# Performance work log

Measured on AMD Instinct MI355X. Metric: run time of the kernel, lower is better.

## Reference

```python
import jax, jax.numpy as jnp
import numpy as np

ADMP = 16  # admp_channel


def _backbone(x, Wc, bc):
    # Conv2d(3->256, k=3, stride=2, pad=1) + ReLU stands in for feature_backbone
    y = jax.lax.conv_general_dilated(x, Wc, window_strides=(2, 2),
                                     padding=((1, 1), (1, 1)),
                                     dimension_numbers=('NCHW', 'OIHW', 'NCHW'))
    return jax.nn.relu(y + bc[None, :, None, None])


def _feature_select(feat, k):
    # AdaptiveMaxPool2d(k, return_indices=True) on feat.sum(1); H,W divisible by k
    B, C, H, W = feat.shape
    bh, bw = H // k, W // k
    resp = feat.sum(1)  # [B,H,W]
    r = resp.reshape(B, k, bh, k, bw).transpose(0, 1, 3, 2, 4).reshape(B, k, k, bh * bw)
    loc = jnp.argmax(r, axis=-1)            # local flat index in each bh*bw block
    lr, lc = loc // bw, loc % bw
    rows = jnp.arange(k)[None, :, None] * bh + lr   # [B,k,k]
    cols = jnp.arange(k)[None, None, :] * bw + lc
    return (rows * W + cols).reshape(B, k * k)      # flat indices into H*W


def _mlp(x, W1, b1, W2, b2):
    # Linear -> ReLU -> (Dropout eval = identity) -> Linear
    return jax.nn.relu(x @ W1 + b1) @ W2 + b2


def reference(xA, xB, Wconv, bconv, W1r, b1r, W2r, b2r, W1c, b1c, W2c, b2c):
    fA = _backbone(xA, Wconv, bconv)  # [B,C,H,W]
    fB = _backbone(xB, Wconv, bconv)
    B, C, H, W = fA.shape
    N = H * W
    idxA = _feature_select(fA, ADMP)                       # [B,K]
    fA_flat = fA.reshape(B, C, N)
    fB_flat = fB.reshape(B, C, N)
    desc = jnp.take_along_axis(fA_flat, idxA[:, None, :], axis=2)  # [B,C,K]
    # ||a-b||^2 = ||a||^2 - 2 a.b + ||b||^2 ; fused batched kNN
    dist = ((desc ** 2).sum(1)[:, :, None]
            - 2.0 * jnp.einsum('bck,bcn->bkn', desc, fB_flat)
            + (fB_flat ** 2).sum(1)[:, None, :])           # [B,K,N]
    minidx = jnp.argmin(dist, axis=-1)                     # [B,K]
    # original uses high (==width here since H==W) for both div and mod
    row_A, col_A = idxA // H, idxA % H
    row_B, col_B = minidx // H, minidx % H
    drow = (row_B - row_A).astype(jnp.float32)             # [B,K]
    dcol = (col_A - col_B).astype(jnp.float32)
    out_drow = _mlp(drow, W1r, b1r, W2r, b2r)              # [B,1]
    out_dcol = _mlp(dcol, W1c, b1c, W2c, b2c)
    return jnp.concatenate([out_drow, out_dcol], axis=1)   # [B,2]


def setup_inputs() -> dict:
    key = jax.random.key(0)
    ks = jax.random.split(key, 8)
    K2 = ADMP * ADMP
    return {
        'xA': jax.random.normal(ks[0], (4, 3, 256, 256), jnp.float32),
        'xB': jax.random.normal(ks[1], (4, 3, 256, 256), jnp.float32),
        'Wconv': jax.random.normal(ks[2], (256, 3, 3, 3), jnp.float32) * 0.1,
        'bconv': jnp.zeros((256,), jnp.float32),
        'W1r': jax.random.normal(ks[3], (K2, K2 // 2), jnp.float32) * 0.05,
        'b1r': jnp.zeros((K2 // 2,), jnp.float32),
        'W2r': jax.random.normal(ks[4], (K2 // 2, 1), jnp.float32) * 0.05,
        'b2r': jnp.zeros((1,), jnp.float32),
        'W1c': jax.random.normal(ks[5], (K2, K2 // 2), jnp.float32) * 0.05,
        'b1c': jnp.zeros((K2 // 2,), jnp.float32),
        'W2c': jax.random.normal(ks[6], (K2 // 2, 1), jnp.float32) * 0.05,
        'b2c': jnp.zeros((1,), jnp.float32),
    }
```

## Files before the change

kernel.cpp:

```cpp
#include <hip/hip_runtime.h>
#include <stdint.h>

constexpr int NB   = 4;
constexpr int CIN  = 3;
constexpr int HIN  = 256;
constexpr int COUT = 256;
constexpr int HF   = 128;
constexpr int NF   = HF * HF;
constexpr int KADM = 16;
constexpr int KK   = KADM * KADM;
constexpr int HID  = 128;
constexpr int DFB  = 65536;
constexpr int PX   = 32;
constexpr int NT   = NF / PX;

typedef unsigned short ushort_t;
typedef __attribute__((ext_vector_type(8))) _Float16 f16x8;
typedef __attribute__((ext_vector_type(2))) __fp16   fp16v2;
typedef __attribute__((ext_vector_type(4))) float    f32x4;

__device__ inline unsigned long long shfl_xor_u64(unsigned long long v, int m) {
    unsigned lo = __shfl_xor((unsigned)v, m, 64);
    unsigned hi = __shfl_xor((unsigned)(v >> 32), m, 64);
    return ((unsigned long long)hi << 32) | lo;
}
__device__ inline unsigned long long u64min(unsigned long long a, unsigned long long b) {
    return a < b ? a : b;
}
__device__ inline ushort_t f16bits(_Float16 h) { return __builtin_bit_cast(ushort_t, h); }

__device__ inline int swz(int pix, int c) {
    return pix * 256 + ((((c >> 3) ^ (pix & 7)) << 3) | (c & 7));
}

__device__ inline int dfoff(int w, int chunk, int j, int lane) {
    return (((w * 8 + chunk) * 4 + j) * 64 + lane) * 8;
}

__global__ __launch_bounds__(256) void prep_kernel(
        const float* __restrict__ W, ushort_t* __restrict__ WFh, ushort_t* __restrict__ WFl)
{
    int co = threadIdx.x;
    int w = co >> 6, j = (co >> 4) & 3, la = co & 15;
    #pragma unroll
    for (int q = 0; q < 32; ++q) {
        float v = (q < 27) ? W[co * 27 + q] : 0.f;
        _Float16 h = (_Float16)v;
        _Float16 l = (_Float16)(v - (float)h);
        int lg = q >> 3, e = q & 7;
        int off = ((w * 4 + j) * 64 + lg * 16 + la) * 8 + e;
        WFh[off] = f16bits(h);
        WFl[off] = f16bits(l);
    }
}

__global__ __launch_bounds__(256) void convA_kernel(
        const float* __restrict__ xA,
        const ushort_t* __restrict__ WFh, const ushort_t* __restrict__ WFl,
        const float* __restrict__ bias, float* __restrict__ resp)
{
    __shared__ float    pS[CIN][3][132];
    __shared__ ushort_t Ah[64][40];
    __shared__ ushort_t Al[64][40];
    __shared__ float    redS[4][64];

    int tile = blockIdx.x;
    int b    = blockIdx.y;
    int oh   = tile >> 1;
    int ow0  = (tile & 1) << 6;
    const float* x = xA + (size_t)b * CIN * HIN * HIN;
    int tid = threadIdx.x;

    for (int i = tid; i < CIN * 3 * 129; i += 256) {
        int ci = i / (3 * 129);
        int r2 = i % (3 * 129);
        int kh = r2 / 129, c = r2 % 129;
        int gr = 2 * oh - 1 + kh, gc = 2 * ow0 - 1 + c;
        float v = 0.f;
        if (gr >= 0 && gr < HIN && gc >= 0 && gc < HIN)
            v = x[(size_t)ci * HIN * HIN + (size_t)gr * HIN + gc];
        pS[ci][kh][c] = v;
    }
    __syncthreads();

    {
        int n = tid >> 2, qg = tid & 3;
        unsigned uh[4], ul[4];
        #pragma unroll
        for (int e2 = 0; e2 < 4; ++e2) {
            ushort_t hh[2], ll[2];
            #pragma unroll
            for (int s = 0; s < 2; ++s) {
                int q = qg * 8 + e2 * 2 + s;
                float v = 0.f;
                if (q < 27) {
                    int ci = q / 9, r = (q % 9) / 3, kw = q % 3;
                    v = pS[ci][r][2 * n + kw];
                }
                _Float16 h = (_Float16)v;
                _Float16 l = (_Float16)(v - (float)h);
                hh[s] = f16bits(h); ll[s] = f16bits(l);
            }
            uh[e2] = (unsigned)hh[0] | ((unsigned)hh[1] << 16);
            ul[e2] = (unsigned)ll[0] | ((unsigned)ll[1] << 16);
        }
        *(uint4*)&Ah[n][qg * 8] = *(uint4*)uh;
        *(uint4*)&Al[n][qg * 8] = *(uint4*)ul;
    }
    __syncthreads();

    int lane = tid & 63, w = tid >> 6;
    int la = lane & 15, lg = lane >> 4;
    int wbase = w * 64;

    float bj[4];
    #pragma unroll
    for (int j = 0; j < 4; ++j) bj[j] = bias[wbase + j * 16 + la];

    f16x8 ah[4], al[4], bh[4], bl[4];
    #pragma unroll
    for (int i = 0; i < 4; ++i) {
        ah[i] = *(const f16x8*)&Ah[i * 16 + la][lg * 8];
        al[i] = *(const f16x8*)&Al[i * 16 + la][lg * 8];
    }
    #pragma unroll
    for (int j = 0; j < 4; ++j) {
        int off = ((w * 4 + j) * 64 + lane) * 8;
        bh[j] = *(const f16x8*)&WFh[off];
        bl[j] = *(const f16x8*)&WFl[off];
    }

    f32x4 acc[4][4];
    #pragma unroll
    for (int i = 0; i < 4; ++i)
        #pragma unroll
        for (int j = 0; j < 4; ++j) acc[i][j] = (f32x4)0.f;

    #pragma unroll
    for (int i = 0; i < 4; ++i)
        #pragma unroll
        for (int j = 0; j < 4; ++j) {
            acc[i][j] = __builtin_amdgcn_mfma_f32_16x16x32_f16(ah[i], bh[j], acc[i][j], 0, 0, 0);
            acc[i][j] = __builtin_amdgcn_mfma_f32_16x16x32_f16(al[i], bh[j], acc[i][j], 0, 0, 0);
            acc[i][j] = __builtin_amdgcn_mfma_f32_16x16x32_f16(ah[i], bl[j], acc[i][j], 0, 0, 0);
        }

    float s[4][4];
    #pragma unroll
    for (int i = 0; i < 4; ++i)
        #pragma unroll
        for (int r = 0; r < 4; ++r) s[i][r] = 0.f;

    #pragma unroll
    for (int i = 0; i < 4; ++i)
        #pragma unroll
        for (int j = 0; j < 4; ++j)
            #pragma unroll
            for (int r = 0; r < 4; ++r)
                s[i][r] += fmaxf(acc[i][j][r] + bj[j], 0.f);

    #pragma unroll
    for (int i = 0; i < 4; ++i)
        #pragma unroll
        for (int r = 0; r < 4; ++r) {
            float v = s[i][r];
            v += __shfl_xor(v, 1, 64);
            v += __shfl_xor(v, 2, 64);
            v += __shfl_xor(v, 4, 64);
            v += __shfl_xor(v, 8, 64);
            s[i][r] = v;
        }
    if (la == 0) {
        #pragma unroll
        for (int i = 0; i < 4; ++i)
            #pragma unroll
            for (int r = 0; r < 4; ++r)
                redS[w][i * 16 + lg * 4 + r] = s[i][r];
    }
    __syncthreads();
    if (tid < 64) {
        float tot = redS[0][tid] + redS[1][tid] + redS[2][tid] + redS[3][tid];
        resp[(size_t)b * NF + oh * HF + ow0 + tid] = tot;
    }
}

__global__ __launch_bounds__(256) void select_kernel(
        const float* __restrict__ resp,
        const float* __restrict__ xA, const float* __restrict__ W,
        const float* __restrict__ bias,
        int* __restrict__ idxA,
        ushort_t* __restrict__ dFh, ushort_t* __restrict__ dFl,
        float* __restrict__ normA)
{
    __shared__ float patch[27];
    __shared__ float red[4];
    __shared__ int   sidx;

    int bk = blockIdx.x;
    int b = bk >> 8, k = bk & 255;
    int t = threadIdx.x;

    if (t < 64) {
        int kr = k >> 4, kc = k & 15;
        int lr = t >> 3, lc = t & 7;
        int row = kr * 8 + lr, col = kc * 8 + lc;
        float bv = resp[(size_t)b * NF + (size_t)row * HF + col];
        int best = t;
        for (int off = 32; off > 0; off >>= 1) {
            float ov = __shfl_down(bv, off, 64);
            int   oi = __shfl_down(best, off, 64);
            if (ov > bv || (ov == bv && oi < best)) { bv = ov; best = oi; }
        }
        if (t == 0) {
            int r = kr * 8 + (best >> 3), c = kc * 8 + (best & 7);
            int idx = r * HF + c;
            idxA[bk] = idx;
            sidx = idx;
        }
    }
    __syncthreads();
    int idx = sidx;
    int oh = idx >> 7, ow = idx & 127;

    if (t < 27) {
        int ci = t / 9, kh = (t % 9) / 3, kw = t % 3;
        int ir = oh * 2 - 1 + kh, ic = ow * 2 - 1 + kw;
        float v = 0.f;
        if (ir >= 0 && ir < HIN && ic >= 0 && ic < HIN)
            v = xA[((size_t)b * CIN + ci) * HIN * HIN + (size_t)ir * HIN + ic];
        patch[t] = v;
    }
    __syncthreads();

    float v = bias[t];
    const float* w = &W[t * 27];
    #pragma unroll
    for (int q = 0; q < 27; ++q) v = fmaf(patch[q], w[q], v);
    v = fmaxf(v, 0.f);

    _Float16 h = (_Float16)v;
    _Float16 l = (_Float16)(v - (float)h);
    {
        int wq = k >> 6, j = (k >> 4) & 3, la = k & 15;
        int chunk = t >> 5, lg = (t >> 3) & 3, e = t & 7;
        int off = b * DFB + dfoff(wq, chunk, j, lg * 16 + la) + e;
        dFh[off] = f16bits(h);
        dFl[off] = f16bits(l);
    }

    float s = v * v;
    for (int off = 32; off > 0; off >>= 1) s += __shfl_down(s, off, 64);
    if ((t & 63) == 0) red[t >> 6] = s;
    __syncthreads();
    if (t == 0) normA[bk] = red[0] + red[1] + red[2] + red[3];
}

__device__ inline void load_desc(const ushort_t* __restrict__ dFh,
                                 const ushort_t* __restrict__ dFl,
                                 int w, int chunk, int lane,
                                 f16x8* bh, f16x8* bl)
{
    #pragma unroll
    for (int j = 0; j < 4; ++j) {
        int off = dfoff(w, chunk, j, lane);
        bh[j] = *(const f16x8*)&dFh[off];
        bl[j] = *(const f16x8*)&dFl[off];
    }
}

__device__ inline void knn_chunk(const ushort_t* __restrict__ fH,
                                 const ushort_t* __restrict__ fL,
                                 int la, int lg, int cc,
                                 const f16x8* bh, const f16x8* bl,
                                 f32x4 (&acc)[2][4])
{
    #pragma unroll
    for (int i = 0; i < 2; ++i) {
        f16x8 ah = *(const f16x8*)&fH[swz(i * 16 + la, cc + lg * 8)];
        f16x8 al = *(const f16x8*)&fL[swz(i * 16 + la, cc + lg * 8)];
        __builtin_amdgcn_s_setprio(1);
        #pragma unroll
        for (int j = 0; j < 4; ++j) {
            acc[i][j] = __builtin_amdgcn_mfma_f32_16x16x32_f16(ah, bh[j], acc[i][j], 0, 0, 0);
            acc[i][j] = __builtin_amdgcn_mfma_f32_16x16x32_f16(al, bh[j], acc[i][j], 0, 0, 0);
            acc[i][j] = __builtin_amdgcn_mfma_f32_16x16x32_f16(ah, bl[j], acc[i][j], 0, 0, 0);
        }
        __builtin_amdgcn_s_setprio(0);
    }
}

__global__ __launch_bounds__(256, 4) void fused_kernel(
        const float* __restrict__ xB,
        const ushort_t* __restrict__ WFh, const ushort_t* __restrict__ WFl,
        const float* __restrict__ bias,
        const ushort_t* __restrict__ dFhg, const ushort_t* __restrict__ dFlg,
        const float* __restrict__ normA,
        unsigned long long* __restrict__ scratch)
{
    __shared__ __align__(16) char smem[2 * PX * 256 * 2];
    __shared__ float redS[4][PX];
    __shared__ float nAS[KK];
    __shared__ float nBS[PX];
    __shared__ float bS[COUT];

    float*    pSp = (float*)smem;
    ushort_t* AhP = (ushort_t*)(smem + 2448);
    ushort_t* AlP = (ushort_t*)(smem + 2448 + 2560);
    ushort_t* fH  = (ushort_t*)smem;
    ushort_t* fL  = (ushort_t*)(smem + PX * 256 * 2);

    int tile = blockIdx.x;
    int b    = blockIdx.y;
    int oh   = tile >> 2;
    int ow0  = (tile & 3) << 5;
    const float* x = xB + (size_t)b * CIN * HIN * HIN;
    int tid = threadIdx.x;

    nAS[tid] = normA[b * KK + tid];
    bS[tid]  = bias[tid];

    for (int i = tid; i < CIN * 3 * 65; i += 256) {
        int ci = i / (3 * 65);
        int r2 = i % (3 * 65);
        int kh = r2 / 65, c = r2 % 65;
        int gr = 2 * oh - 1 + kh, gc = 2 * ow0 - 1 + c;
        float v = 0.f;
        if (gr >= 0 && gr < HIN && gc >= 0 && gc < HIN)
            v = x[(size_t)ci * HIN * HIN + (size_t)gr * HIN + gc];
        pSp[ci * 204 + kh * 68 + c] = v;
    }
    __syncthreads();

    {
        int n = tid >> 3, qg = tid & 7;
        ushort_t hh[4], ll[4];
        #pragma unroll
        for (int s = 0; s < 4; ++s) {
            int q = qg * 4 + s;
            float v = 0.f;
            if (q < 27) {
                int ci = q / 9, r = (q % 9) / 3, kw = q % 3;
                v = pSp[ci * 204 + r * 68 + 2 * n + kw];
            }
            _Float16 h = (_Float16)v;
            _Float16 l = (_Float16)(v - (float)h);
            hh[s] = f16bits(h); ll[s] = f16bits(l);
        }
        unsigned lo, hi;
        lo = (unsigned)hh[0] | ((unsigned)hh[1] << 16);
        hi = (unsigned)hh[2] | ((unsigned)hh[3] << 16);
        *(uint2*)&AhP[n * 40 + qg * 4] = make_uint2(lo, hi);
        lo = (unsigned)ll[0] | ((unsigned)ll[1] << 16);
        hi = (unsigned)ll[2] | ((unsigned)ll[3] << 16);
        *(uint2*)&AlP[n * 40 + qg * 4] = make_uint2(lo, hi);
    }
    __syncthreads();

    int lane = tid & 63, w = tid >> 6;
    int la = lane & 15, lg = lane >> 4;
    int wbase = w * 64;

    f16x8 wah[4], wal[4], pbh[2], pbl[2];
    #pragma unroll
    for (int j = 0; j < 4; ++j) {
        int off = ((w * 4 + j) * 64 + lane) * 8;
        wah[j] = *(const f16x8*)&WFh[off];
        wal[j] = *(const f16x8*)&WFl[off];
    }
    #pragma unroll
    for (int i = 0; i < 2; ++i) {
        pbh[i] = *(const f16x8*)&AhP[(i * 16 + la) * 40 + lg * 8];
        pbl[i] = *(const f16x8*)&AlP[(i * 16 + la) * 40 + lg * 8];
    }

    f32x4 cacc[4][2];
    #pragma unroll
    for (int j = 0; j < 4; ++j)
        #pragma unroll
        for (int i = 0; i < 2; ++i) cacc[j][i] = (f32x4)0.f;

    #pragma unroll
    for (int j = 0; j < 4; ++j)
        #pragma unroll
        for (int i = 0; i < 2; ++i) {
            cacc[j][i] = __builtin_amdgcn_mfma_f32_16x16x32_f16(wah[j], pbh[i], cacc[j][i], 0, 0, 0);
            cacc[j][i] = __builtin_amdgcn_mfma_f32_16x16x32_f16(wal[j], pbh[i], cacc[j][i], 0, 0, 0);
            cacc[j][i] = __builtin_amdgcn_mfma_f32_16x16x32_f16(wah[j], pbl[i], cacc[j][i], 0, 0, 0);
        }

    __syncthreads();

    float s2[2] = {0.f, 0.f};
    #pragma unroll
    for (int j = 0; j < 4; ++j) {
        f32x4 b4 = *(const f32x4*)&bS[wbase + j * 16 + lg * 4];
        int chunk = (wbase + j * 16 + lg * 4) >> 3;
        int within = (lg & 1) * 4;
        #pragma unroll
        for (int i = 0; i < 2; ++i) {
            int pix = i * 16 + la;
            float v0 = fmaxf(cacc[j][i][0] + b4[0], 0.f);
            float v1 = fmaxf(cacc[j][i][1] + b4[1], 0.f);
            float v2 = fmaxf(cacc[j][i][2] + b4[2], 0.f);
            float v3 = fmaxf(cacc[j][i][3] + b4[3], 0.f);
            s2[i] += v0 * v0 + v1 * v1 + v2 * v2 + v3 * v3;
            fp16v2 h01 = __builtin_amdgcn_cvt_pkrtz(v0, v1);
            fp16v2 h23 = __builtin_amdgcn_cvt_pkrtz(v2, v3);
            fp16v2 l01 = __builtin_amdgcn_cvt_pkrtz(v0 - (float)h01[0], v1 - (float)h01[1]);
            fp16v2 l23 = __builtin_amdgcn_cvt_pkrtz(v2 - (float)h23[0], v3 - (float)h23[1]);
            int base = pix * 256 + ((chunk ^ (pix & 7)) << 3) + within;
            *(uint2*)&fH[base] = make_uint2(__builtin_bit_cast(unsigned, h01),
                                            __builtin_bit_cast(unsigned, h23));
            *(uint2*)&fL[base] = make_uint2(__builtin_bit_cast(unsigned, l01),
                                            __builtin_bit_cast(unsigned, l23));
        }
    }

    const ushort_t* dFh = dFhg + (size_t)b * DFB;
    const ushort_t* dFl = dFlg + (size_t)b * DFB;
    f16x8 bhA[4], blA[4], bhB[4], blB[4];
    load_desc(dFh, dFl, w, 0, lane, bhA, blA);
    load_desc(dFh, dFl, w, 1, lane, bhB, blB);

    #pragma unroll
    for (int i = 0; i < 2; ++i) {
        float v = s2[i];
        v += __shfl_xor(v, 16, 64);
        v += __shfl_xor(v, 32, 64);
        if (lg == 0) redS[w][i * 16 + la] = v;
    }
    __syncthreads();
    if (tid < PX) nBS[tid] = redS[0][tid] + redS[1][tid] + redS[2][tid] + redS[3][tid];
    __syncthreads();

    f32x4 acc[2][4];
    #pragma unroll
    for (int i = 0; i < 2; ++i)
        #pragma unroll
        for (int j = 0; j < 4; ++j) acc[i][j] = (f32x4)0.f;

    knn_chunk(fH, fL, la, lg, 0, bhA, blA, acc);
    load_desc(dFh, dFl, w, 2, lane, bhA, blA);
    knn_chunk(fH, fL, la, lg, 32, bhB, blB, acc);
    load_desc(dFh, dFl, w, 3, lane, bhB, blB);
    knn_chunk(fH, fL, la, lg, 64, bhA, blA, acc);
    load_desc(dFh, dFl, w, 4, lane, bhA, blA);
    knn_chunk(fH, fL, la, lg, 96, bhB, blB, acc);
    load_desc(dFh, dFl, w, 5, lane, bhB, blB);
    knn_chunk(fH, fL, la, lg, 128, bhA, blA, acc);
    load_desc(dFh, dFl, w, 6, lane, bhA, blA);
    knn_chunk(fH, fL, la, lg, 160, bhB, blB, acc);
    load_desc(dFh, dFl, w, 7, lane, bhB, blB);
    knn_chunk(fH, fL, la, lg, 192, bhA, blA, acc);
    knn_chunk(fH, fL, la, lg, 224, bhB, blB, acc);

    float nBv[2][4];
    #pragma unroll
    for (int i = 0; i < 2; ++i) {
        f32x4 t4 = *(const f32x4*)&nBS[i * 16 + lg * 4];
        nBv[i][0] = t4[0]; nBv[i][1] = t4[1]; nBv[i][2] = t4[2]; nBv[i][3] = t4[3];
    }
    int n0 = tile * PX;
    unsigned long long bestj[4];
    #pragma unroll
    for (int j = 0; j < 4; ++j) {
        int kl = wbase + j * 16 + la;
        float nAv = nAS[kl];
        unsigned long long best = ~0ull;
        #pragma unroll
        for (int i = 0; i < 2; ++i)
            #pragma unroll
            for (int r = 0; r < 4; ++r) {
                int n = n0 + i * 16 + lg * 4 + r;
                float d = fmaf(-2.f, acc[i][j][r], nAv) + nBv[i][r];
                unsigned u = __float_as_uint(d);
                u = (u & 0x80000000u) ? ~u : (u | 0x80000000u);
                unsigned long long key = ((unsigned long long)u << 32) | (unsigned)n;
                best = u64min(best, key);
            }
        best = u64min(best, shfl_xor_u64(best, 16));
        best = u64min(best, shfl_xor_u64(best, 32));
        bestj[j] = best;
    }
    unsigned long long key = (lg == 0) ? bestj[0] : (lg == 1) ? bestj[1]
                           : (lg == 2) ? bestj[2] : bestj[3];
    int klw = wbase + lg * 16 + la;
    scratch[((size_t)b * NT + tile) * KK + klw] = key;
}

__global__ __launch_bounds__(256) void reduce_kernel(
        const unsigned long long* __restrict__ scratch, int* __restrict__ minN)
{
    __shared__ unsigned long long part[8][32];
    int g = blockIdx.x;
    int b = blockIdx.y;
    int t = threadIdx.x;
    int ts = t >> 5, kk = t & 31;
    int k = g * 32 + kk;

    unsigned long long best = ~0ull;
    #pragma unroll 4
    for (int m = 0; m < NT / 8; ++m) {
        int tile = m * 8 + ts;
        best = u64min(best, scratch[((size_t)b * NT + tile) * KK + k]);
    }
    part[ts][kk] = best;
    __syncthreads();
    if (t < 32) {
        unsigned long long x = part[0][t];
        #pragma unroll
        for (int p = 1; p < 8; ++p) x = u64min(x, part[p][t]);
        minN[b * KK + g * 32 + t] = (int)(x & 0xffffffffULL);
    }
}

__global__ __launch_bounds__(128) void mlp_kernel(
        const int* __restrict__ idxA, const int* __restrict__ minN,
        const float* __restrict__ W1r, const float* __restrict__ b1r,
        const float* __restrict__ W2r, const float* __restrict__ b2r,
        const float* __restrict__ W1c, const float* __restrict__ b1c,
        const float* __restrict__ W2c, const float* __restrict__ b2c,
        float* __restrict__ out)
{
    __shared__ float xS[KK];
    __shared__ float red[2];
    int blk = blockIdx.x;
    int b = blk >> 1, which = blk & 1;
    int t = threadIdx.x;

    for (int k = t; k < KK; k += 128) {
        int ia = idxA[b * KK + k];
        int nn = minN[b * KK + k];
        int rowA = ia >> 7, colA = ia & 127;
        int rowB = nn >> 7, colB = nn & 127;
        xS[k] = (which == 0) ? (float)(rowB - rowA) : (float)(colA - colB);
    }
    __syncthreads();

    const float* W1 = which ? W1c : W1r;
    const float* b1 = which ? b1c : b1r;
    const float* W2 = which ? W2c : W2r;
    const float* b2 = which ? b2c : b2r;

    float h = b1[t];
    for (int k = 0; k < KK; ++k) h = fmaf(xS[k], W1[k * HID + t], h);
    h = fmaxf(h, 0.f);
    float pv = h * W2[t];
    for (int off = 32; off > 0; off >>= 1) pv += __shfl_down(pv, off, 64);
    if ((t & 63) == 0) red[t >> 6] = pv;
    __syncthreads();
    if (t == 0) out[b * 2 + which] = red[0] + red[1] + b2[0];
}

extern "C" void kernel_launch(void* const* d_in, const int* in_sizes, int n_in,
                              void* d_out, int out_size, void* d_ws, size_t ws_size,
                              hipStream_t stream)
{
    const float* xA  = (const float*)d_in[0];
    const float* xB  = (const float*)d_in[1];
    const float* Wc  = (const float*)d_in[2];
    const float* bc  = (const float*)d_in[3];
    const float* W1r = (const float*)d_in[4];
    const float* b1r = (const float*)d_in[5];
    const float* W2r = (const float*)d_in[6];
    const float* b2r = (const float*)d_in[7];
    const float* W1c = (const float*)d_in[8];
    const float* b1c = (const float*)d_in[9];
    const float* W2c = (const float*)d_in[10];
    const float* b2c = (const float*)d_in[11];
    float* out = (float*)d_out;

    char* ws = (char*)d_ws;
    unsigned long long* scratch = (unsigned long long*)ws; ws += (size_t)NB * KK * NT * 8;
    int*   idxA   = (int*)ws;      ws += (size_t)NB * KK * 4;
    int*   minN   = (int*)ws;      ws += (size_t)NB * KK * 4;
    float* normA  = (float*)ws;    ws += (size_t)NB * KK * 4;
    float* resp   = (float*)ws;    ws += (size_t)NB * NF * 4;
    ushort_t* dFh = (ushort_t*)ws; ws += (size_t)NB * DFB * 2;
    ushort_t* dFl = (ushort_t*)ws; ws += (size_t)NB * DFB * 2;
    ushort_t* WFh = (ushort_t*)ws; ws += (size_t)COUT * 32 * 2;
    ushort_t* WFl = (ushort_t*)ws; ws += (size_t)COUT * 32 * 2;

    prep_kernel  <<<1, 256, 0, stream>>>(Wc, WFh, WFl);
    convA_kernel <<<dim3(256, NB), 256, 0, stream>>>(xA, WFh, WFl, bc, resp);
    select_kernel<<<NB * KK, 256, 0, stream>>>(resp, xA, Wc, bc, idxA, dFh, dFl, normA);
    fused_kernel <<<dim3(NT, NB), 256, 0, stream>>>(xB, WFh, WFl, bc, dFh, dFl,
                                                    normA, scratch);
    reduce_kernel<<<dim3(8, NB), 256, 0, stream>>>(scratch, minN);
    mlp_kernel   <<<8, 128, 0, stream>>>(idxA, minN,
                                         W1r, b1r, W2r, b2r,
                                         W1c, b1c, W2c, b2c, out);
}
```

Before: 69.96 us.

## Replace scratch argmin reduction with global atomicMin and halve convA grid

Result: slower. 72.04 us (+3.0%).

```diff
diff --git a/kernel.cpp b/kernel.cpp
--- a/kernel.cpp
+++ b/kernel.cpp
@@ -19,11 +19,6 @@
 typedef __attribute__((ext_vector_type(2))) __fp16   fp16v2;
 typedef __attribute__((ext_vector_type(4))) float    f32x4;
 
-__device__ inline unsigned long long shfl_xor_u64(unsigned long long v, int m) {
-    unsigned lo = __shfl_xor((unsigned)v, m, 64);
-    unsigned hi = __shfl_xor((unsigned)(v >> 32), m, 64);
-    return ((unsigned long long)hi << 32) | lo;
-}
 __device__ inline unsigned long long u64min(unsigned long long a, unsigned long long b) {
     return a < b ? a : b;
 }
@@ -64,123 +59,126 @@
     __shared__ ushort_t Al[64][40];
     __shared__ float    redS[4][64];
 
-    int tile = blockIdx.x;
-    int b    = blockIdx.y;
-    int oh   = tile >> 1;
-    int ow0  = (tile & 1) << 6;
+    int b = blockIdx.y;
     const float* x = xA + (size_t)b * CIN * HIN * HIN;
     int tid = threadIdx.x;
-
-    for (int i = tid; i < CIN * 3 * 129; i += 256) {
-        int ci = i / (3 * 129);
-        int r2 = i % (3 * 129);
-        int kh = r2 / 129, c = r2 % 129;
-        int gr = 2 * oh - 1 + kh, gc = 2 * ow0 - 1 + c;
-        float v = 0.f;
-        if (gr >= 0 && gr < HIN && gc >= 0 && gc < HIN)
-            v = x[(size_t)ci * HIN * HIN + (size_t)gr * HIN + gc];
-        pS[ci][kh][c] = v;
-    }
-    __syncthreads();
-
-    {
-        int n = tid >> 2, qg = tid & 3;
-        unsigned uh[4], ul[4];
-        #pragma unroll
-        for (int e2 = 0; e2 < 4; ++e2) {
-            ushort_t hh[2], ll[2];
-            #pragma unroll
-            for (int s = 0; s < 2; ++s) {
-                int q = qg * 8 + e2 * 2 + s;
-                float v = 0.f;
-                if (q < 27) {
-                    int ci = q / 9, r = (q % 9) / 3, kw = q % 3;
-                    v = pS[ci][r][2 * n + kw];
-                }
-                _Float16 h = (_Float16)v;
-                _Float16 l = (_Float16)(v - (float)h);
-                hh[s] = f16bits(h); ll[s] = f16bits(l);
-            }
-            uh[e2] = (unsigned)hh[0] | ((unsigned)hh[1] << 16);
-            ul[e2] = (unsigned)ll[0] | ((unsigned)ll[1] << 16);
-        }
-        *(uint4*)&Ah[n][qg * 8] = *(uint4*)uh;
-        *(uint4*)&Al[n][qg * 8] = *(uint4*)ul;
-    }
-    __syncthreads();
-
     int lane = tid & 63, w = tid >> 6;
     int la = lane & 15, lg = lane >> 4;
     int wbase = w * 64;
 
     float bj[4];
-    #pragma unroll
-    for (int j = 0; j < 4; ++j) bj[j] = bias[wbase + j * 16 + la];
-
-    f16x8 ah[4], al[4], bh[4], bl[4];
-    #pragma unroll
-    for (int i = 0; i < 4; ++i) {
-        ah[i] = *(const f16x8*)&Ah[i * 16 + la][lg * 8];
-        al[i] = *(const f16x8*)&Al[i * 16 + la][lg * 8];
-    }
+    f16x8 bh[4], bl[4];
     #pragma unroll
     for (int j = 0; j < 4; ++j) {
+        bj[j] = bias[wbase + j * 16 + la];
         int off = ((w * 4 + j) * 64 + lane) * 8;
         bh[j] = *(const f16x8*)&WFh[off];
         bl[j] = *(const f16x8*)&WFl[off];
     }
 
-    f32x4 acc[4][4];
-    #pragma unroll
-    for (int i = 0; i < 4; ++i)
-        #pragma unroll
-        for (int j = 0; j < 4; ++j) acc[i][j] = (f32x4)0.f;
-
-    #pragma unroll
-    for (int i = 0; i < 4; ++i)
-        #pragma unroll
-        for (int j = 0; j < 4; ++j) {
-            acc[i][j] = __builtin_amdgcn_mfma_f32_16x16x32_f16(ah[i], bh[j], acc[i][j], 0, 0, 0);
-            acc[i][j] = __builtin_amdgcn_mfma_f32_16x16x32_f16(al[i], bh[j], acc[i][j], 0, 0, 0);
-            acc[i][j] = __builtin_amdgcn_mfma_f32_16x16x32_f16(ah[i], bl[j], acc[i][j], 0, 0, 0);
-        }
-
-    float s[4][4];
-    #pragma unroll
-    for (int i = 0; i < 4; ++i)
-        #pragma unroll
-        for (int r = 0; r < 4; ++r) s[i][r] = 0.f;
-
-    #pragma unroll
-    for (int i = 0; i < 4; ++i)
-        #pragma unroll
-        for (int j = 0; j < 4; ++j)
-            #pragma unroll
-            for (int r = 0; r < 4; ++r)
-                s[i][r] += fmaxf(acc[i][j][r] + bj[j], 0.f);
-
-    #pragma unroll
-    for (int i = 0; i < 4; ++i)
-        #pragma unroll
-        for (int r = 0; r < 4; ++r) {
-            float v = s[i][r];
-            v += __shfl_xor(v, 1, 64);
-            v += __shfl_xor(v, 2, 64);
-            v += __shfl_xor(v, 4, 64);
-            v += __shfl_xor(v, 8, 64);
-            s[i][r] = v;
-        }
-    if (la == 0) {
+    for (int t2 = 0; t2 < 2; ++t2) {
+        int tile = blockIdx.x * 2 + t2;
+        int oh  = tile >> 1;
+        int ow0 = (tile & 1) << 6;
+
+        if (t2) __syncthreads();
+        for (int i = tid; i < CIN * 3 * 129; i += 256) {
+            int ci = i / (3 * 129);
+            int r2 = i % (3 * 129);
+            int kh = r2 / 129, c = r2 % 129;
+            int gr = 2 * oh - 1 + kh, gc = 2 * ow0 - 1 + c;
+            float v = 0.f;
+            if (gr >= 0 && gr < HIN && gc >= 0 && gc < HIN)
+                v = x[(size_t)ci * HIN * HIN + (size_t)gr * HIN + gc];
+            pS[ci][kh][c] = v;
+        }
+        __syncthreads();
+
+        {
+            int n = tid >> 2, qg = tid & 3;
+            unsigned uh[4], ul[4];
+            #pragma unroll
+            for (int e2 = 0; e2 < 4; ++e2) {
+                ushort_t hh[2], ll[2];
+                #pragma unroll
+                for (int s = 0; s < 2; ++s) {
+                    int q = qg * 8 + e2 * 2 + s;
+                    float v = 0.f;
+                    if (q < 27) {
+                        int ci = q / 9, r = (q % 9) / 3, kw = q % 3;
+                        v = pS[ci][r][2 * n + kw];
+                    }
+                    _Float16 h = (_Float16)v;
+                    _Float16 l = (_Float16)(v - (float)h);
+                    hh[s] = f16bits(h); ll[s] = f16bits(l);
+                }
+                uh[e2] = (unsigned)hh[0] | ((unsigned)hh[1] << 16);
+                ul[e2] = (unsigned)ll[0] | ((unsigned)ll[1] << 16);
+            }
+            *(uint4*)&Ah[n][qg * 8] = *(uint4*)uh;
+            *(uint4*)&Al[n][qg * 8] = *(uint4*)ul;
+        }
+        __syncthreads();
+
+        f16x8 ah[4], al[4];
+        #pragma unroll
+        for (int i = 0; i < 4; ++i) {
+            ah[i] = *(const f16x8*)&Ah[i * 16 + la][lg * 8];
+            al[i] = *(const f16x8*)&Al[i * 16 + la][lg * 8];
+        }
+
+        f32x4 acc[4][4];
         #pragma unroll
         for (int i = 0; i < 4; ++i)
             #pragma unroll
-            for (int r = 0; r < 4; ++r)
-                redS[w][i * 16 + lg * 4 + r] = s[i][r];
-    }
-    __syncthreads();
-    if (tid < 64) {
-        float tot = redS[0][tid] + redS[1][tid] + redS[2][tid] + redS[3][tid];
-        resp[(size_t)b * NF + oh * HF + ow0 + tid] = tot;
+            for (int j = 0; j < 4; ++j) acc[i][j] = (f32x4)0.f;
+
+        #pragma unroll
+        for (int i = 0; i < 4; ++i)
+            #pragma unroll
+            for (int j = 0; j < 4; ++j) {
+                acc[i][j] = __builtin_amdgcn_mfma_f32_16x16x32_f16(ah[i], bh[j], acc[i][j], 0, 0, 0);
+                acc[i][j] = __builtin_amdgcn_mfma_f32_16x16x32_f16(al[i], bh[j], acc[i][j], 0, 0, 0);
+                acc[i][j] = __builtin_amdgcn_mfma_f32_16x16x32_f16(ah[i], bl[j], acc[i][j], 0, 0, 0);
+            }
+
+        float s[4][4];
+        #pragma unroll
+        for (int i = 0; i < 4; ++i)
+            #pragma unroll
+            for (int r = 0; r < 4; ++r) s[i][r] = 0.f;
+
+        #pragma unroll
+        for (int i = 0; i < 4; ++i)
+            #pragma unroll
+            for (int j = 0; j < 4; ++j)
+                #pragma unroll
+                for (int r = 0; r < 4; ++r)
+                    s[i][r] += fmaxf(acc[i][j][r] + bj[j], 0.f);
+
+        #pragma unroll
+        for (int i = 0; i < 4; ++i)
+            #pragma unroll
+            for (int r = 0; r < 4; ++r) {
+                float v = s[i][r];
+                v += __shfl_xor(v, 1, 64);
+                v += __shfl_xor(v, 2, 64);
+                v += __shfl_xor(v, 4, 64);
+                v += __shfl_xor(v, 8, 64);
+                s[i][r] = v;
+            }
+        if (la == 0) {
+            #pragma unroll
+            for (int i = 0; i < 4; ++i)
+                #pragma unroll
+                for (int r = 0; r < 4; ++r)
+                    redS[w][i * 16 + lg * 4 + r] = s[i][r];
+        }
+        __syncthreads();
+        if (tid < 64) {
+            float tot = redS[0][tid] + redS[1][tid] + redS[2][tid] + redS[3][tid];
+            resp[(size_t)b * NF + oh * HF + ow0 + tid] = tot;
+        }
     }
 }
 
@@ -295,7 +293,7 @@
         const float* __restrict__ bias,
         const ushort_t* __restrict__ dFhg, const ushort_t* __restrict__ dFlg,
         const float* __restrict__ normA,
-        unsigned long long* __restrict__ scratch)
+        unsigned long long* __restrict__ packed)
 {
     __shared__ __align__(16) char smem[2 * PX * 256 * 2];
     __shared__ float redS[4][PX];
@@ -461,61 +459,43 @@
         nBv[i][0] = t4[0]; nBv[i][1] = t4[1]; nBv[i][2] = t4[2]; nBv[i][3] = t4[3];
     }
     int n0 = tile * PX;
-    unsigned long long bestj[4];
+    float bd[4];
+    int   bn[4];
     #pragma unroll
     for (int j = 0; j < 4; ++j) {
         int kl = wbase + j * 16 + la;
         float nAv = nAS[kl];
-        unsigned long long best = ~0ull;
+        float bestd = 3.4e38f;
+        int   bestn = 0;
         #pragma unroll
         for (int i = 0; i < 2; ++i)
             #pragma unroll
             for (int r = 0; r < 4; ++r) {
                 int n = n0 + i * 16 + lg * 4 + r;
                 float d = fmaf(-2.f, acc[i][j][r], nAv) + nBv[i][r];
-                unsigned u = __float_as_uint(d);
-                u = (u & 0x80000000u) ? ~u : (u | 0x80000000u);
-                unsigned long long key = ((unsigned long long)u << 32) | (unsigned)n;
-                best = u64min(best, key);
+                if (d < bestd) { bestd = d; bestn = n; }
             }
-        best = u64min(best, shfl_xor_u64(best, 16));
-        best = u64min(best, shfl_xor_u64(best, 32));
-        bestj[j] = best;
-    }
-    unsigned long long key = (lg == 0) ? bestj[0] : (lg == 1) ? bestj[1]
-                           : (lg == 2) ? bestj[2] : bestj[3];
+        #pragma unroll
+        for (int off = 16; off <= 32; off <<= 1) {
+            float od = __shfl_xor(bestd, off, 64);
+            int   on = __shfl_xor(bestn, off, 64);
+            bool take = (od < bestd) || (od == bestd && on < bestn);
+            bestd = take ? od : bestd;
+            bestn = take ? on : bestn;
+        }
+        bd[j] = bestd; bn[j] = bestn;
+    }
+    float fd = (lg == 0) ? bd[0] : (lg == 1) ? bd[1] : (lg == 2) ? bd[2] : bd[3];
+    int   fn = (lg == 0) ? bn[0] : (lg == 1) ? bn[1] : (lg == 2) ? bn[2] : bn[3];
+    unsigned u = __float_as_uint(fd);
+    u = (u & 0x80000000u) ? ~u : (u | 0x80000000u);
+    unsigned long long key = ((unsigned long long)u << 32) | (unsigned)fn;
     int klw = wbase + lg * 16 + la;
-    scratch[((size_t)b * NT + tile) * KK + klw] = key;
-}
-
-__global__ __launch_bounds__(256) void reduce_kernel(
-        const unsigned long long* __restrict__ scratch, int* __restrict__ minN)
-{
-    __shared__ unsigned long long part[8][32];
-    int g = blockIdx.x;
-    int b = blockIdx.y;
-    int t = threadIdx.x;
-    int ts = t >> 5, kk = t & 31;
-    int k = g * 32 + kk;
-
-    unsigned long long best = ~0ull;
-    #pragma unroll 4
-    for (int m = 0; m < NT / 8; ++m) {
-        int tile = m * 8 + ts;
-        best = u64min(best, scratch[((size_t)b * NT + tile) * KK + k]);
-    }
-    part[ts][kk] = best;
-    __syncthreads();
-    if (t < 32) {
-        unsigned long long x = part[0][t];
-        #pragma unroll
-        for (int p = 1; p < 8; ++p) x = u64min(x, part[p][t]);
-        minN[b * KK + g * 32 + t] = (int)(x & 0xffffffffULL);
-    }
+    atomicMin(&packed[b * KK + klw], key);
 }
 
 __global__ __launch_bounds__(128) void mlp_kernel(
-        const int* __restrict__ idxA, const int* __restrict__ minN,
+        const int* __restrict__ idxA, const unsigned long long* __restrict__ packed,
         const float* __restrict__ W1r, const float* __restrict__ b1r,
         const float* __restrict__ W2r, const float* __restrict__ b2r,
         const float* __restrict__ W1c, const float* __restrict__ b1c,
@@ -530,7 +510,7 @@
 
     for (int k = t; k < KK; k += 128) {
         int ia = idxA[b * KK + k];
-        int nn = minN[b * KK + k];
+        int nn = (int)(packed[b * KK + k] & 0xffffffffULL);
         int rowA = ia >> 7, colA = ia & 127;
         int rowB = nn >> 7, colB = nn & 127;
         xS[k] = (which == 0) ? (float)(rowB - rowA) : (float)(colA - colB);
@@ -571,9 +551,8 @@
     float* out = (float*)d_out;
 
     char* ws = (char*)d_ws;
-    unsigned long long* scratch = (unsigned long long*)ws; ws += (size_t)NB * KK * NT * 8;
+    unsigned long long* packed = (unsigned long long*)ws; ws += (size_t)NB * KK * 8;
     int*   idxA   = (int*)ws;      ws += (size_t)NB * KK * 4;
-    int*   minN   = (int*)ws;      ws += (size_t)NB * KK * 4;
     float* normA  = (float*)ws;    ws += (size_t)NB * KK * 4;
     float* resp   = (float*)ws;    ws += (size_t)NB * NF * 4;
     ushort_t* dFh = (ushort_t*)ws; ws += (size_t)NB * DFB * 2;
@@ -581,13 +560,14 @@
     ushort_t* WFh = (ushort_t*)ws; ws += (size_t)COUT * 32 * 2;
     ushort_t* WFl = (ushort_t*)ws; ws += (size_t)COUT * 32 * 2;
 
+    hipMemsetAsync(packed, 0xFF, (size_t)NB * KK * 8, stream);
+
     prep_kernel  <<<1, 256, 0, stream>>>(Wc, WFh, WFl);
-    convA_kernel <<<dim3(256, NB), 256, 0, stream>>>(xA, WFh, WFl, bc, resp);
+    convA_kernel <<<dim3(128, NB), 256, 0, stream>>>(xA, WFh, WFl, bc, resp);
     select_kernel<<<NB * KK, 256, 0, stream>>>(resp, xA, Wc, bc, idxA, dFh, dFl, normA);
     fused_kernel <<<dim3(NT, NB), 256, 0, stream>>>(xB, WFh, WFl, bc, dFh, dFl,
-                                                    normA, scratch);
-    reduce_kernel<<<dim3(8, NB), 256, 0, stream>>>(scratch, minN);
-    mlp_kernel   <<<8, 128, 0, stream>>>(idxA, minN,
+                                                    normA, packed);
+    mlp_kernel   <<<8, 128, 0, stream>>>(idxA, packed,
                                          W1r, b1r, W2r, b2r,
                                          W1c, b1c, W2c, b2c, out);
 }
```
